# Kernel optimization log

Measured on AMD Instinct MI355X. Metric: run time of the kernel, lower is better.

The kernel has to match this reference:

```python
import jax, jax.numpy as jnp
import numpy as np

N, E, F_IN = 12288, 196608, 1433


def setup_inputs() -> dict:
    key = jax.random.key(0)
    ks = jax.random.split(key, 11)
    inp = {
        "x": jax.random.normal(ks[0], (N, F_IN), dtype=jnp.float32),
        "edge_index": jax.random.randint(ks[1], (2, E), 0, N, dtype=jnp.int64),
        "W1": jax.random.normal(ks[2], (F_IN, 32), dtype=jnp.float32) * 0.02,
        "b1": jnp.zeros((32,), dtype=jnp.float32),
        "Wl": jax.random.normal(ks[3], (32, 16), dtype=jnp.float32) * 0.1,
        "bl": jnp.zeros((16,), dtype=jnp.float32),
        "Wr": jax.random.normal(ks[4], (32, 16), dtype=jnp.float32) * 0.1,
        "br": jnp.zeros((16,), dtype=jnp.float32),
        "W3": jax.random.normal(ks[5], (16, 7), dtype=jnp.float32) * 0.1,
        "b3": jnp.zeros((7,), dtype=jnp.float32),
    }
    return inp


def reference(x, edge_index, W1, b1, Wl, bl, Wr, br, W3, b3):
    n = x.shape[0]
    loops = jnp.arange(n, dtype=edge_index.dtype)
    row = jnp.concatenate([edge_index[0], loops])  # [E+N]
    col = jnp.concatenate([edge_index[1], loops])

    # ---- GCN layer: dense symmetric-normalized adjacency (faithful to original) ----
    # degree computed over the col index of self-looped edges
    deg = jnp.zeros((n,), dtype=x.dtype).at[col].add(1.0)
    dis = jnp.where(deg > 0, deg ** -0.5, 0.0)  # inf -> 0 guard
    A = jnp.zeros((n, n), dtype=x.dtype).at[row, col].add(1.0)  # dense A-hat
    A_norm = dis[:, None] * A * dis[None, :]  # D^-1/2 A D^-1/2
    h = (A_norm @ x) @ W1 + b1
    h = jax.nn.relu(h)  # [N, 32]

    # ---- GraphSAGE layer: mean over neighbors j with edge (i -> j) ----
    src, dst = edge_index[0], edge_index[1]
    agg_sum = jax.ops.segment_sum(h[dst], src, num_segments=n)  # [N, 32]
    cnt = jax.ops.segment_sum(jnp.ones((src.shape[0],), dtype=h.dtype), src, num_segments=n)
    agg = jnp.where(cnt[:, None] > 0, agg_sum / jnp.maximum(cnt, 1.0)[:, None], 0.0)
    out = jax.nn.relu(h @ Wl + bl + agg @ Wr + br)  # [N, 16]
    out = out / (jnp.linalg.norm(out, axis=1, keepdims=True) + 1e-6)

    # ---- head: linear + dropout(eval: identity) + softmax ----
    logits = out @ W3 + b3  # [N, 7]
    return jax.nn.softmax(logits, axis=1)
```

## Files before the change

kernel.cpp:

```cpp
#include <hip/hip_runtime.h>
#include <hip/hip_bf16.h>
#include <math.h>

#define GN 12288
#define GE 196608
#define GK 1433
#define GC 32
#define CAP 64
#define NGRP 192
#define GEMMB 768
#define EDGEB 768
#define PACKB 24
#define ZEROB 96
#define XSTR 516

typedef __attribute__((ext_vector_type(8))) short bf16x8;
typedef __attribute__((ext_vector_type(4))) float f32x4;
typedef float f32x4a __attribute__((ext_vector_type(4), aligned(4)));

static __device__ inline unsigned short f2bf(float f) {
    unsigned u = __float_as_uint(f);
    return (unsigned short)((u + 0x7fffu + ((u >> 16) & 1u)) >> 16);
}
static __device__ inline float bf2f(unsigned short h) {
    return __uint_as_float(((unsigned)h) << 16);
}
static __device__ inline unsigned short f2bf_hw(float f) {
    return __builtin_bit_cast(unsigned short, __float2bfloat16(f));
}

__global__ __launch_bounds__(256) void prep_kernel(const float* __restrict__ W1,
                                                   unsigned* __restrict__ zbuf,
                                                   unsigned short* __restrict__ Whb,
                                                   unsigned short* __restrict__ Wlb) {
    int t = threadIdx.x, b = blockIdx.x;
    if (b < PACKB) {
        int idx = b * 256 + t;
        int g = idx >> 5, c = idx & 31;
        bf16x8 vh, vl;
        #pragma unroll
        for (int j = 0; j < 8; ++j) {
            int k = g * 8 + j;
            float f = (k < GK) ? W1[(size_t)k * GC + c] : 0.f;
            unsigned short hh = f2bf(f);
            vh[j] = (short)hh;
            vl[j] = (short)f2bf(f - bf2f(hh));
        }
        *(bf16x8*)(Whb + (size_t)idx * 8) = vh;
        *(bf16x8*)(Wlb + (size_t)idx * 8) = vl;
    } else {
        int idx = (b - PACKB) * 256 + t;
        zbuf[idx] = 0u;
    }
}

__global__ __launch_bounds__(256) void fused_kernel(const float* __restrict__ x,
                                                    const int* __restrict__ ei,
                                                    const unsigned short* __restrict__ Whb,
                                                    const unsigned short* __restrict__ Wlb,
                                                    float* __restrict__ xw,
                                                    unsigned* __restrict__ cnt,
                                                    unsigned* __restrict__ deg,
                                                    unsigned* __restrict__ adjF) {
    int t = threadIdx.x, bid = blockIdx.x;

    if (bid >= GEMMB) {
        int e = (bid - GEMMB) * 256 + t;
        int src = ei[e];
        int dst = ei[GE + e];
        unsigned pos = atomicAdd(&cnt[src], 1u);
        if (pos < CAP) adjF[(unsigned)src * CAP + pos] = (unsigned)dst;
        atomicAdd(&deg[dst], 1u);
        return;
    }

    __shared__ __align__(16) float xs[16][XSTR];
    int lane = t & 63, w = t >> 6;
    int quad = lane >> 4, l15 = lane & 15;
    const float* xb = x + (size_t)bid * 16 * GK;
    f32x4 acc0 = {}, acc1 = {};

    int r0 = t >> 7;
    int pos = t & 127;
    f32x4 g0, g1, g2, g3, g4, g5, g6, g7;

#define LOADG(K0) { \
    const float* pp = xb + (size_t)r0 * GK + (K0) + pos * 4; \
    g0 = *(const f32x4a*)(pp); \
    g1 = *(const f32x4a*)(pp + 2 * GK); \
    g2 = *(const f32x4a*)(pp + 4 * GK); \
    g3 = *(const f32x4a*)(pp + 6 * GK); \
    g4 = *(const f32x4a*)(pp + 8 * GK); \
    g5 = *(const f32x4a*)(pp + 10 * GK); \
    g6 = *(const f32x4a*)(pp + 12 * GK); \
    g7 = *(const f32x4a*)(pp + 14 * GK); }

#define LG1(DST, ROFF, PP, KB) { \
    const float* q_ = (PP) + (size_t)(ROFF) * GK; \
    if ((KB) + 4 <= GK) DST = *(const f32x4a*)q_; \
    else { \
        DST[0] = ((KB) + 0 < GK) ? q_[0] : 0.f; \
        DST[1] = ((KB) + 1 < GK) ? q_[1] : 0.f; \
        DST[2] = ((KB) + 2 < GK) ? q_[2] : 0.f; \
        DST[3] = ((KB) + 3 < GK) ? q_[3] : 0.f; } }

#define LOADG_TAIL(K0) { \
    const float* pp = xb + (size_t)r0 * GK + (K0) + pos * 4; \
    int kb = (K0) + pos * 4; \
    LG1(g0, 0, pp, kb)  LG1(g1, 2, pp, kb)  LG1(g2, 4, pp, kb)  LG1(g3, 6, pp, kb) \
    LG1(g4, 8, pp, kb)  LG1(g5, 10, pp, kb) LG1(g6, 12, pp, kb) LG1(g7, 14, pp, kb) }

#define STOREL() { \
    float* lp = &xs[r0][pos * 4]; \
    *(f32x4*)(lp)              = g0; \
    *(f32x4*)(lp + 2 * XSTR)   = g1; \
    *(f32x4*)(lp + 4 * XSTR)   = g2; \
    *(f32x4*)(lp + 6 * XSTR)   = g3; \
    *(f32x4*)(lp + 8 * XSTR)   = g4; \
    *(f32x4*)(lp + 10 * XSTR)  = g5; \
    *(f32x4*)(lp + 12 * XSTR)  = g6; \
    *(f32x4*)(lp + 14 * XSTR)  = g7; }

#define COMPUTE(S) { \
    _Pragma("unroll") \
    for (int c = 0; c < 4; ++c) { \
        int kl = w * 128 + c * 32 + quad * 8; \
        const float* ap = &xs[l15][kl]; \
        f32x4 x0 = *(const f32x4*)ap; \
        f32x4 x1 = *(const f32x4*)(ap + 4); \
        bf16x8 ah, al; \
        _Pragma("unroll") for (int j = 0; j < 4; ++j) { \
            unsigned short hh = f2bf_hw(x0[j]); \
            ah[j] = (short)hh; al[j] = (short)f2bf_hw(x0[j] - bf2f(hh)); } \
        _Pragma("unroll") for (int j = 0; j < 4; ++j) { \
            unsigned short hh = f2bf_hw(x1[j]); \
            ah[4 + j] = (short)hh; al[4 + j] = (short)f2bf_hw(x1[j] - bf2f(hh)); } \
        int gg = (S) * 64 + w * 16 + c * 4 + quad; \
        bf16x8 H0 = *(const bf16x8*)(Whb + (size_t)gg * 256 + l15 * 8); \
        bf16x8 H1 = *(const bf16x8*)(Whb + (size_t)gg * 256 + 128 + l15 * 8); \
        bf16x8 L0 = *(const bf16x8*)(Wlb + (size_t)gg * 256 + l15 * 8); \
        bf16x8 L1 = *(const bf16x8*)(Wlb + (size_t)gg * 256 + 128 + l15 * 8); \
        acc0 = __builtin_amdgcn_mfma_f32_16x16x32_bf16(ah, H0, acc0, 0, 0, 0); \
        acc1 = __builtin_amdgcn_mfma_f32_16x16x32_bf16(ah, H1, acc1, 0, 0, 0); \
        acc0 = __builtin_amdgcn_mfma_f32_16x16x32_bf16(ah, L0, acc0, 0, 0, 0); \
        acc1 = __builtin_amdgcn_mfma_f32_16x16x32_bf16(ah, L1, acc1, 0, 0, 0); \
        acc0 = __builtin_amdgcn_mfma_f32_16x16x32_bf16(al, H0, acc0, 0, 0, 0); \
        acc1 = __builtin_amdgcn_mfma_f32_16x16x32_bf16(al, H1, acc1, 0, 0, 0); \
    } }

    LOADG(0);
    STOREL();
    __syncthreads();
    LOADG(512);
    COMPUTE(0);
    __syncthreads();
    STOREL();
    __syncthreads();
    LOADG_TAIL(1024);
    COMPUTE(1);
    __syncthreads();
    STOREL();
    __syncthreads();
    COMPUTE(2);
    __syncthreads();

    float (*red)[16][32] = (float (*)[16][32])(&xs[0][0]);
    #pragma unroll
    for (int i = 0; i < 4; ++i) {
        red[w][quad * 4 + i][l15] = acc0[i];
        red[w][quad * 4 + i][16 + l15] = acc1[i];
    }
    __syncthreads();
    int rr0 = t >> 5, cc0 = t & 31;
    float s0 = red[0][rr0][cc0] + red[1][rr0][cc0] + red[2][rr0][cc0] + red[3][rr0][cc0];
    int rr1 = rr0 + 8;
    float s1 = red[0][rr1][cc0] + red[1][rr1][cc0] + red[2][rr1][cc0] + red[3][rr1][cc0];
    xw[(size_t)bid * 512 + t] = s0;
    xw[(size_t)bid * 512 + 256 + t] = s1;
}

__global__ __launch_bounds__(256) void gcn_kernel(const float* __restrict__ xw,
                                                  const unsigned* __restrict__ deg,
                                                  const unsigned* __restrict__ cnt,
                                                  const unsigned* __restrict__ adjF,
                                                  const float* __restrict__ b1,
                                                  float* __restrict__ h) {
    int w = threadIdx.x >> 6;
    int lane = threadIdx.x & 63;
    int i = blockIdx.x * 4 + w;
    int f = lane & 31, half = lane >> 5;
    unsigned cl = min(cnt[i], (unsigned)CAP);
    const unsigned* ai = adjF + (unsigned)i * CAP;
    float acc = 0.f;
    for (unsigned j = half; j < cl; j += 8) {
        unsigned lim = cl - 1;
        unsigned j1 = j + 2, j2 = j + 4, j3 = j + 6;
        unsigned d0 = ai[j];
        unsigned d1 = ai[min(j1, lim)];
        unsigned d2 = ai[min(j2, lim)];
        unsigned d3 = ai[min(j3, lim)];
        float m1 = j1 < cl ? 1.f : 0.f;
        float m2 = j2 < cl ? 1.f : 0.f;
        float m3 = j3 < cl ? 1.f : 0.f;
        acc += xw[(size_t)d0 * GC + f] * rsqrtf((float)(deg[d0] + 1u));
        acc += m1 * xw[(size_t)d1 * GC + f] * rsqrtf((float)(deg[d1] + 1u));
        acc += m2 * xw[(size_t)d2 * GC + f] * rsqrtf((float)(deg[d2] + 1u));
        acc += m3 * xw[(size_t)d3 * GC + f] * rsqrtf((float)(deg[d3] + 1u));
    }
    acc += __shfl_xor(acc, 32, 64);
    float disi = rsqrtf((float)(deg[i] + 1u));
    float v = b1[f] + disi * (disi * xw[(size_t)i * GC + f] + acc);
    if (half == 0) h[(size_t)i * GC + f] = fmaxf(v, 0.f);
}

__global__ __launch_bounds__(256) void sage_kernel(const float* __restrict__ h,
                                                   const unsigned* __restrict__ cnt,
                                                   const unsigned* __restrict__ adjF,
                                                   const float* __restrict__ Wl,
                                                   const float* __restrict__ bl,
                                                   const float* __restrict__ Wr,
                                                   const float* __restrict__ br,
                                                   const float* __restrict__ W3,
                                                   const float* __restrict__ b3,
                                                   float* __restrict__ out) {
    __shared__ float sh[4][64];
    __shared__ float so[4][16];
    int w = threadIdx.x >> 6, lane = threadIdx.x & 63;
    int i = blockIdx.x * 4 + w;
    int f = lane & 31, half = lane >> 5;
    unsigned ci = cnt[i];
    unsigned cl = min(ci, (unsigned)CAP);
    const unsigned* ai = adjF + (unsigned)i * CAP;
    float acc = 0.f;
    for (unsigned j = half; j < cl; j += 8) {
        unsigned lim = cl - 1;
        unsigned j1 = j + 2, j2 = j + 4, j3 = j + 6;
        unsigned d0 = ai[j];
        unsigned d1 = ai[min(j1, lim)];
        unsigned d2 = ai[min(j2, lim)];
        unsigned d3 = ai[min(j3, lim)];
        float m1 = j1 < cl ? 1.f : 0.f;
        float m2 = j2 < cl ? 1.f : 0.f;
        float m3 = j3 < cl ? 1.f : 0.f;
        acc += h[(size_t)d0 * GC + f];
        acc += m1 * h[(size_t)d1 * GC + f];
        acc += m2 * h[(size_t)d2 * GC + f];
        acc += m3 * h[(size_t)d3 * GC + f];
    }
    acc += __shfl_xor(acc, 32, 64);
    float agg = ci ? acc / (float)ci : 0.f;
    float hv = h[(size_t)i * GC + f];
    if (half == 0) { sh[w][f] = hv; sh[w][32 + f] = agg; }
    __syncthreads();
    int c = lane;
    float hid = 0.f;
    if (c < 16) {
        hid = bl[c] + br[c];
        #pragma unroll
        for (int ff = 0; ff < 32; ++ff)
            hid += sh[w][ff] * Wl[ff * 16 + c] + sh[w][32 + ff] * Wr[ff * 16 + c];
        hid = fmaxf(hid, 0.f);
    }
    float n2 = hid * hid;
    n2 += __shfl_xor(n2, 1, 64);
    n2 += __shfl_xor(n2, 2, 64);
    n2 += __shfl_xor(n2, 4, 64);
    n2 += __shfl_xor(n2, 8, 64);
    float o = hid / (sqrtf(n2) + 1e-6f);
    if (c < 16) so[w][c] = o;
    __syncthreads();
    float logit = -INFINITY;
    if (lane < 7) {
        logit = b3[lane];
        #pragma unroll
        for (int cc = 0; cc < 16; ++cc) logit += so[w][cc] * W3[cc * 7 + lane];
    }
    float m = logit;
    m = fmaxf(m, __shfl_xor(m, 1, 64));
    m = fmaxf(m, __shfl_xor(m, 2, 64));
    m = fmaxf(m, __shfl_xor(m, 4, 64));
    float e = expf(logit - m);
    float s = e;
    s += __shfl_xor(s, 1, 64);
    s += __shfl_xor(s, 2, 64);
    s += __shfl_xor(s, 4, 64);
    if (lane < 7) out[(size_t)i * 7 + lane] = e / s;
}

extern "C" void kernel_launch(void* const* d_in, const int* in_sizes, int n_in,
                              void* d_out, int out_size, void* d_ws, size_t ws_size,
                              hipStream_t stream) {
    const float* x  = (const float*)d_in[0];
    const int*   ei = (const int*)d_in[1];
    const float* W1 = (const float*)d_in[2];
    const float* b1 = (const float*)d_in[3];
    const float* Wl = (const float*)d_in[4];
    const float* bl = (const float*)d_in[5];
    const float* Wr = (const float*)d_in[6];
    const float* br = (const float*)d_in[7];
    const float* W3 = (const float*)d_in[8];
    const float* b3 = (const float*)d_in[9];
    float* out = (float*)d_out;

    char* ws = (char*)d_ws;
    const size_t S = (size_t)GN * GC * 4;
    float*    xw   = (float*)(ws);
    unsigned* cnt  = (unsigned*)(ws + S);
    unsigned* deg  = cnt + GN;
    float*    h    = (float*)(deg + GN);
    unsigned* adjF = (unsigned*)((char*)h + S);
    unsigned short* Whb = (unsigned short*)((char*)adjF + (size_t)GN * CAP * 4);
    unsigned short* Wlb = Whb + (size_t)NGRP * GC * 8;

    prep_kernel<<<PACKB + ZEROB, 256, 0, stream>>>(W1, cnt, Whb, Wlb);
    fused_kernel<<<GEMMB + EDGEB, 256, 0, stream>>>(x, ei, Whb, Wlb, xw, cnt, deg, adjF);
    gcn_kernel<<<GN / 4, 256, 0, stream>>>(xw, deg, cnt, adjF, b1, h);
    sage_kernel<<<GN / 4, 256, 0, stream>>>(h, cnt, adjF, Wl, bl, Wr, br, W3, b3, out);
}
```

Measured before the change: 154.1 us.

## Fuse edge, GEMM, GCN and SAGE stages into one cooperative kernel with grid syncs

```diff
diff --git a/kernel.cpp b/kernel.cpp
--- a/kernel.cpp
+++ b/kernel.cpp
@@ -1,6 +1,9 @@
 #include <hip/hip_runtime.h>
+#include <hip/hip_cooperative_groups.h>
 #include <hip/hip_bf16.h>
 #include <math.h>
+
+namespace cg = cooperative_groups;
 
 #define GN 12288
 #define GE 196608
@@ -13,6 +16,7 @@
 #define PACKB 24
 #define ZEROB 96
 #define XSTR 516
+#define NBLK 768
 
 typedef __attribute__((ext_vector_type(8))) short bf16x8;
 typedef __attribute__((ext_vector_type(4))) float f32x4;
@@ -29,57 +33,29 @@
     return __builtin_bit_cast(unsigned short, __float2bfloat16(f));
 }
 
-__global__ __launch_bounds__(256) void prep_kernel(const float* __restrict__ W1,
-                                                   unsigned* __restrict__ zbuf,
-                                                   unsigned short* __restrict__ Whb,
-                                                   unsigned short* __restrict__ Wlb) {
-    int t = threadIdx.x, b = blockIdx.x;
-    if (b < PACKB) {
-        int idx = b * 256 + t;
-        int g = idx >> 5, c = idx & 31;
-        bf16x8 vh, vl;
-        #pragma unroll
-        for (int j = 0; j < 8; ++j) {
-            int k = g * 8 + j;
-            float f = (k < GK) ? W1[(size_t)k * GC + c] : 0.f;
-            unsigned short hh = f2bf(f);
-            vh[j] = (short)hh;
-            vl[j] = (short)f2bf(f - bf2f(hh));
-        }
-        *(bf16x8*)(Whb + (size_t)idx * 8) = vh;
-        *(bf16x8*)(Wlb + (size_t)idx * 8) = vl;
-    } else {
-        int idx = (b - PACKB) * 256 + t;
-        zbuf[idx] = 0u;
-    }
-}
-
-__global__ __launch_bounds__(256) void fused_kernel(const float* __restrict__ x,
-                                                    const int* __restrict__ ei,
-                                                    const unsigned short* __restrict__ Whb,
-                                                    const unsigned short* __restrict__ Wlb,
-                                                    float* __restrict__ xw,
-                                                    unsigned* __restrict__ cnt,
-                                                    unsigned* __restrict__ deg,
-                                                    unsigned* __restrict__ adjF) {
-    int t = threadIdx.x, bid = blockIdx.x;
-
-    if (bid >= GEMMB) {
-        int e = (bid - GEMMB) * 256 + t;
-        int src = ei[e];
-        int dst = ei[GE + e];
-        unsigned pos = atomicAdd(&cnt[src], 1u);
-        if (pos < CAP) adjF[(unsigned)src * CAP + pos] = (unsigned)dst;
-        atomicAdd(&deg[dst], 1u);
-        return;
-    }
-
-    __shared__ __align__(16) float xs[16][XSTR];
+
+static __device__ __forceinline__ void edge_body(int e, const int* __restrict__ ei,
+                                                 unsigned* __restrict__ cnt,
+                                                 unsigned* __restrict__ deg,
+                                                 unsigned* __restrict__ adjF) {
+    int src = ei[e];
+    int dst = ei[GE + e];
+    unsigned pos = atomicAdd(&cnt[src], 1u);
+    if (pos < CAP) adjF[(unsigned)src * CAP + pos] = (unsigned)dst;
+    atomicAdd(&deg[dst], 1u);
+}
+
+static __device__ __forceinline__ void gemm_body(int bid, int t,
+                                                 const float* __restrict__ x,
+                                                 const unsigned short* __restrict__ Whb,
+                                                 const unsigned short* __restrict__ Wlb,
+                                                 float* __restrict__ xw,
+                                                 float* smem) {
     int lane = t & 63, w = t >> 6;
     int quad = lane >> 4, l15 = lane & 15;
+    float (*xs)[XSTR] = (float (*)[XSTR])smem;
     const float* xb = x + (size_t)bid * 16 * GK;
     f32x4 acc0 = {}, acc1 = {};
-
     int r0 = t >> 7;
     int pos = t & 127;
     f32x4 g0, g1, g2, g3, g4, g5, g6, g7;
@@ -164,7 +140,7 @@
     COMPUTE(2);
     __syncthreads();
 
-    float (*red)[16][32] = (float (*)[16][32])(&xs[0][0]);
+    float (*red)[16][32] = (float (*)[16][32])smem;
     #pragma unroll
     for (int i = 0; i < 4; ++i) {
         red[w][quad * 4 + i][l15] = acc0[i];
@@ -177,17 +153,20 @@
     float s1 = red[0][rr1][cc0] + red[1][rr1][cc0] + red[2][rr1][cc0] + red[3][rr1][cc0];
     xw[(size_t)bid * 512 + t] = s0;
     xw[(size_t)bid * 512 + 256 + t] = s1;
-}
-
-__global__ __launch_bounds__(256) void gcn_kernel(const float* __restrict__ xw,
-                                                  const unsigned* __restrict__ deg,
-                                                  const unsigned* __restrict__ cnt,
-                                                  const unsigned* __restrict__ adjF,
-                                                  const float* __restrict__ b1,
-                                                  float* __restrict__ h) {
-    int w = threadIdx.x >> 6;
-    int lane = threadIdx.x & 63;
-    int i = blockIdx.x * 4 + w;
+#undef LOADG
+#undef LG1
+#undef LOADG_TAIL
+#undef STOREL
+#undef COMPUTE
+}
+
+static __device__ __forceinline__ void gcn_body(int i, int lane,
+                                                const float* __restrict__ xw,
+                                                const unsigned* __restrict__ deg,
+                                                const unsigned* __restrict__ cnt,
+                                                const unsigned* __restrict__ adjF,
+                                                const float* __restrict__ b1,
+                                                float* __restrict__ h) {
     int f = lane & 31, half = lane >> 5;
     unsigned cl = min(cnt[i], (unsigned)CAP);
     const unsigned* ai = adjF + (unsigned)i * CAP;
@@ -213,20 +192,18 @@
     if (half == 0) h[(size_t)i * GC + f] = fmaxf(v, 0.f);
 }
 
-__global__ __launch_bounds__(256) void sage_kernel(const float* __restrict__ h,
-                                                   const unsigned* __restrict__ cnt,
-                                                   const unsigned* __restrict__ adjF,
-                                                   const float* __restrict__ Wl,
-                                                   const float* __restrict__ bl,
-                                                   const float* __restrict__ Wr,
-                                                   const float* __restrict__ br,
-                                                   const float* __restrict__ W3,
-                                                   const float* __restrict__ b3,
-                                                   float* __restrict__ out) {
-    __shared__ float sh[4][64];
-    __shared__ float so[4][16];
-    int w = threadIdx.x >> 6, lane = threadIdx.x & 63;
-    int i = blockIdx.x * 4 + w;
+static __device__ __forceinline__ void sage_body(int i, int w, int lane,
+                                                 float (*sh)[64], float (*so)[16],
+                                                 const float* __restrict__ h,
+                                                 const unsigned* __restrict__ cnt,
+                                                 const unsigned* __restrict__ adjF,
+                                                 const float* __restrict__ Wl,
+                                                 const float* __restrict__ bl,
+                                                 const float* __restrict__ Wr,
+                                                 const float* __restrict__ br,
+                                                 const float* __restrict__ W3,
+                                                 const float* __restrict__ b3,
+                                                 float* __restrict__ out) {
     int f = lane & 31, half = lane >> 5;
     unsigned ci = cnt[i];
     unsigned cl = min(ci, (unsigned)CAP);
@@ -279,12 +256,130 @@
     m = fmaxf(m, __shfl_xor(m, 1, 64));
     m = fmaxf(m, __shfl_xor(m, 2, 64));
     m = fmaxf(m, __shfl_xor(m, 4, 64));
-    float e = expf(logit - m);
-    float s = e;
+    float ev = expf(logit - m);
+    float s = ev;
     s += __shfl_xor(s, 1, 64);
     s += __shfl_xor(s, 2, 64);
     s += __shfl_xor(s, 4, 64);
-    if (lane < 7) out[(size_t)i * 7 + lane] = e / s;
+    if (lane < 7) out[(size_t)i * 7 + lane] = ev / s;
+}
+
+
+__global__ __launch_bounds__(256) void prep_kernel(const float* __restrict__ W1,
+                                                   unsigned* __restrict__ zbuf,
+                                                   unsigned short* __restrict__ Whb,
+                                                   unsigned short* __restrict__ Wlb) {
+    int t = threadIdx.x, b = blockIdx.x;
+    if (b < PACKB) {
+        int idx = b * 256 + t;
+        int g = idx >> 5, c = idx & 31;
+        bf16x8 vh, vl;
+        #pragma unroll
+        for (int j = 0; j < 8; ++j) {
+            int k = g * 8 + j;
+            float f = (k < GK) ? W1[(size_t)k * GC + c] : 0.f;
+            unsigned short hh = f2bf(f);
+            vh[j] = (short)hh;
+            vl[j] = (short)f2bf(f - bf2f(hh));
+        }
+        *(bf16x8*)(Whb + (size_t)idx * 8) = vh;
+        *(bf16x8*)(Wlb + (size_t)idx * 8) = vl;
+    } else {
+        int idx = (b - PACKB) * 256 + t;
+        zbuf[idx] = 0u;
+    }
+}
+
+__global__ __launch_bounds__(256) void mega3_kernel(
+    const float* __restrict__ x,
+    const int* __restrict__ ei,
+    const unsigned short* __restrict__ Whb,
+    const unsigned short* __restrict__ Wlb,
+    float* __restrict__ xw,
+    unsigned* __restrict__ cnt,
+    unsigned* __restrict__ deg,
+    unsigned* __restrict__ adjF,
+    const float* __restrict__ b1,
+    float* __restrict__ h,
+    const float* __restrict__ Wl,
+    const float* __restrict__ bl,
+    const float* __restrict__ Wr,
+    const float* __restrict__ br,
+    const float* __restrict__ W3,
+    const float* __restrict__ b3,
+    float* __restrict__ out)
+{
+    cg::grid_group grid = cg::this_grid();
+    int t = threadIdx.x, bid = blockIdx.x;
+    int lane = t & 63, w = t >> 6;
+    __shared__ __align__(16) float smem[16 * XSTR];
+
+    edge_body(bid * 256 + t, ei, cnt, deg, adjF);
+    gemm_body(bid, t, x, Whb, Wlb, xw, smem);
+
+    __threadfence_system();
+    grid.sync();
+    __threadfence_system();
+
+    #pragma unroll
+    for (int n = 0; n < 4; ++n)
+        gcn_body(bid * 16 + n * 4 + w, lane, xw, deg, cnt, adjF, b1, h);
+
+    __threadfence_system();
+    grid.sync();
+    __threadfence_system();
+
+    {
+        float (*sh)[64] = (float (*)[64])smem;
+        float (*so)[16] = (float (*)[16])(smem + 256);
+        for (int n = 0; n < 4; ++n)
+            sage_body(bid * 16 + n * 4 + w, w, lane, sh, so,
+                      h, cnt, adjF, Wl, bl, Wr, br, W3, b3, out);
+    }
+}
+
+__global__ __launch_bounds__(256) void fused_kernel(const float* __restrict__ x,
+                                                    const int* __restrict__ ei,
+                                                    const unsigned short* __restrict__ Whb,
+                                                    const unsigned short* __restrict__ Wlb,
+                                                    float* __restrict__ xw,
+                                                    unsigned* __restrict__ cnt,
+                                                    unsigned* __restrict__ deg,
+                                                    unsigned* __restrict__ adjF) {
+    int t = threadIdx.x, bid = blockIdx.x;
+    if (bid >= GEMMB) {
+        edge_body((bid - GEMMB) * 256 + t, ei, cnt, deg, adjF);
+        return;
+    }
+    __shared__ __align__(16) float smem[16 * XSTR];
+    gemm_body(bid, t, x, Whb, Wlb, xw, smem);
+}
+
+__global__ __launch_bounds__(256) void gcn_kernel(const float* __restrict__ xw,
+                                                  const unsigned* __restrict__ deg,
+                                                  const unsigned* __restrict__ cnt,
+                                                  const unsigned* __restrict__ adjF,
+                                                  const float* __restrict__ b1,
+                                                  float* __restrict__ h) {
+    int w = threadIdx.x >> 6, lane = threadIdx.x & 63;
+    gcn_body(blockIdx.x * 4 + w, lane, xw, deg, cnt, adjF, b1, h);
+}
+
+__global__ __launch_bounds__(256) void sage_kernel(const float* __restrict__ h,
+                                                   const unsigned* __restrict__ cnt,
+                                                   const unsigned* __restrict__ adjF,
+                                                   const float* __restrict__ Wl,
+                                                   const float* __restrict__ bl,
+                                                   const float* __restrict__ Wr,
+                                                   const float* __restrict__ br,
+                                                   const float* __restrict__ W3,
+                                                   const float* __restrict__ b3,
+                                                   float* __restrict__ out) {
+    __shared__ float sh[4][64];
+    __shared__ float so[4][16];
+    int w = threadIdx.x >> 6, lane = threadIdx.x & 63;
+    sage_body(blockIdx.x * 4 + w, w, lane, sh, so,
+              h, cnt, adjF, Wl, bl, Wr, br, W3, b3, out);
 }
 
 extern "C" void kernel_launch(void* const* d_in, const int* in_sizes, int n_in,
@@ -313,7 +408,20 @@
     unsigned short* Wlb = Whb + (size_t)NGRP * GC * 8;
 
     prep_kernel<<<PACKB + ZEROB, 256, 0, stream>>>(W1, cnt, Whb, Wlb);
-    fused_kernel<<<GEMMB + EDGEB, 256, 0, stream>>>(x, ei, Whb, Wlb, xw, cnt, deg, adjF);
-    gcn_kernel<<<GN / 4, 256, 0, stream>>>(xw, deg, cnt, adjF, b1, h);
-    sage_kernel<<<GN / 4, 256, 0, stream>>>(h, cnt, adjF, Wl, bl, Wr, br, W3, b3, out);
-}
+
+    void* args[] = {
+        (void*)&x, (void*)&ei, (void*)&Whb, (void*)&Wlb,
+        (void*)&xw, (void*)&cnt, (void*)&deg, (void*)&adjF,
+        (void*)&b1, (void*)&h,
+        (void*)&Wl, (void*)&bl, (void*)&Wr, (void*)&br,
+        (void*)&W3, (void*)&b3, (void*)&out
+    };
+    hipError_t err = hipLaunchCooperativeKernel((void*)mega3_kernel, dim3(NBLK),
+                                                dim3(256), args, 0, stream);
+    if (err != hipSuccess) {
+        (void)hipGetLastError();
+        fused_kernel<<<GEMMB + EDGEB, 256, 0, stream>>>(x, ei, Whb, Wlb, xw, cnt, deg, adjF);
+        gcn_kernel<<<GN / 4, 256, 0, stream>>>(xw, deg, cnt, adjF, b1, h);
+        sage_kernel<<<GN / 4, 256, 0, stream>>>(h, cnt, adjF, Wl, bl, Wr, br, W3, b3, out);
+    }
+}
```

Result: slower. 571.0 us (+270.4%).

## Aggregate edge counts in LDS histograms before global atomics

Applied to the files above, without the earlier changes.

```diff
diff --git a/kernel.cpp b/kernel.cpp
--- a/kernel.cpp
+++ b/kernel.cpp
@@ -9,7 +9,8 @@
 #define CAP 64
 #define NGRP 192
 #define GEMMB 768
-#define EDGEB 768
+#define NEDGE 8
+#define EPB   24576
 #define PACKB 24
 #define ZEROB 96
 #define XSTR 516
@@ -64,22 +65,47 @@
                                                     unsigned* __restrict__ adjF) {
     int t = threadIdx.x, bid = blockIdx.x;
 
-    if (bid >= GEMMB) {
-        int e = (bid - GEMMB) * 256 + t;
-        int src = ei[e];
-        int dst = ei[GE + e];
-        unsigned pos = atomicAdd(&cnt[src], 1u);
-        if (pos < CAP) adjF[(unsigned)src * CAP + pos] = (unsigned)dst;
-        atomicAdd(&deg[dst], 1u);
+    if (bid < NEDGE) {
+        __shared__ unsigned lc[GN];
+        __shared__ unsigned short base16[GN];
+        int e0 = bid * EPB;
+        for (int i = t; i < GN; i += 256) lc[i] = 0u;
+        __syncthreads();
+        for (int k = t; k < EPB; k += 256)
+            atomicAdd(&lc[ei[e0 + k]], 1u);
+        __syncthreads();
+        for (int i = t; i < GN; i += 256) {
+            unsigned c = lc[i];
+            if (c) base16[i] = (unsigned short)atomicAdd(&cnt[i], c);
+        }
+        __syncthreads();
+        for (int i = t; i < GN; i += 256) lc[i] = 0u;
+        __syncthreads();
+        for (int k = t; k < EPB; k += 256) {
+            int s = ei[e0 + k];
+            int d = ei[GE + e0 + k];
+            unsigned p = (unsigned)base16[s] + atomicAdd(&lc[s], 1u);
+            if (p < CAP) adjF[(unsigned)s * CAP + p] = (unsigned)d;
+        }
+        __syncthreads();
+        for (int i = t; i < GN; i += 256) lc[i] = 0u;
+        __syncthreads();
+        for (int k = t; k < EPB; k += 256)
+            atomicAdd(&lc[ei[GE + e0 + k]], 1u);
+        __syncthreads();
+        for (int i = t; i < GN; i += 256) {
+            unsigned c = lc[i];
+            if (c) atomicAdd(&deg[i], c);
+        }
         return;
     }
 
+    int gb = bid - NEDGE;
     __shared__ __align__(16) float xs[16][XSTR];
     int lane = t & 63, w = t >> 6;
     int quad = lane >> 4, l15 = lane & 15;
-    const float* xb = x + (size_t)bid * 16 * GK;
+    const float* xb = x + (size_t)gb * 16 * GK;
     f32x4 acc0 = {}, acc1 = {};
-
     int r0 = t >> 7;
     int pos = t & 127;
     f32x4 g0, g1, g2, g3, g4, g5, g6, g7;
@@ -175,8 +201,8 @@
     float s0 = red[0][rr0][cc0] + red[1][rr0][cc0] + red[2][rr0][cc0] + red[3][rr0][cc0];
     int rr1 = rr0 + 8;
     float s1 = red[0][rr1][cc0] + red[1][rr1][cc0] + red[2][rr1][cc0] + red[3][rr1][cc0];
-    xw[(size_t)bid * 512 + t] = s0;
-    xw[(size_t)bid * 512 + 256 + t] = s1;
+    xw[(size_t)gb * 512 + t] = s0;
+    xw[(size_t)gb * 512 + 256 + t] = s1;
 }
 
 __global__ __launch_bounds__(256) void gcn_kernel(const float* __restrict__ xw,
@@ -313,7 +339,7 @@
     unsigned short* Wlb = Whb + (size_t)NGRP * GC * 8;
 
     prep_kernel<<<PACKB + ZEROB, 256, 0, stream>>>(W1, cnt, Whb, Wlb);
-    fused_kernel<<<GEMMB + EDGEB, 256, 0, stream>>>(x, ei, Whb, Wlb, xw, cnt, deg, adjF);
+    fused_kernel<<<NEDGE + GEMMB, 256, 0, stream>>>(x, ei, Whb, Wlb, xw, cnt, deg, adjF);
     gcn_kernel<<<GN / 4, 256, 0, stream>>>(xw, deg, cnt, adjF, b1, h);
     sage_kernel<<<GN / 4, 256, 0, stream>>>(h, cnt, adjF, Wl, bl, Wr, br, W3, b3, out);
 }
```

Result: slower. 247.9 us (+60.9%).

## Double-buffer LDS staging of x in the GEMM with smaller K chunks

Applied to the files above, without the earlier changes.

```diff
diff --git a/kernel.cpp b/kernel.cpp
--- a/kernel.cpp
+++ b/kernel.cpp
@@ -12,7 +12,7 @@
 #define EDGEB 768
 #define PACKB 24
 #define ZEROB 96
-#define XSTR 516
+#define XSTR2 260
 
 typedef __attribute__((ext_vector_type(8))) short bf16x8;
 typedef __attribute__((ext_vector_type(4))) float f32x4;
@@ -74,26 +74,22 @@
         return;
     }
 
-    __shared__ __align__(16) float xs[16][XSTR];
+    __shared__ __align__(16) float smem[2 * 16 * XSTR2];
+    float (*xs)[16][XSTR2] = (float (*)[16][XSTR2])smem;
     int lane = t & 63, w = t >> 6;
     int quad = lane >> 4, l15 = lane & 15;
     const float* xb = x + (size_t)bid * 16 * GK;
     f32x4 acc0 = {}, acc1 = {};
-
-    int r0 = t >> 7;
-    int pos = t & 127;
-    f32x4 g0, g1, g2, g3, g4, g5, g6, g7;
-
-#define LOADG(K0) { \
-    const float* pp = xb + (size_t)r0 * GK + (K0) + pos * 4; \
-    g0 = *(const f32x4a*)(pp); \
-    g1 = *(const f32x4a*)(pp + 2 * GK); \
-    g2 = *(const f32x4a*)(pp + 4 * GK); \
-    g3 = *(const f32x4a*)(pp + 6 * GK); \
-    g4 = *(const f32x4a*)(pp + 8 * GK); \
-    g5 = *(const f32x4a*)(pp + 10 * GK); \
-    g6 = *(const f32x4a*)(pp + 12 * GK); \
-    g7 = *(const f32x4a*)(pp + 14 * GK); }
+    int r0w = t >> 6;
+    int posc = t & 63;
+    f32x4 gA0, gA1, gA2, gA3, gB0, gB1, gB2, gB3;
+
+#define LOADG(G0, G1, G2, G3, S) { \
+    const float* pp = xb + (size_t)r0w * GK + (S) * 256 + posc * 4; \
+    G0 = *(const f32x4a*)(pp); \
+    G1 = *(const f32x4a*)(pp + 4 * GK); \
+    G2 = *(const f32x4a*)(pp + 8 * GK); \
+    G3 = *(const f32x4a*)(pp + 12 * GK); }
 
 #define LG1(DST, ROFF, PP, KB) { \
     const float* q_ = (PP) + (size_t)(ROFF) * GK; \
@@ -104,28 +100,23 @@
         DST[2] = ((KB) + 2 < GK) ? q_[2] : 0.f; \
         DST[3] = ((KB) + 3 < GK) ? q_[3] : 0.f; } }
 
-#define LOADG_TAIL(K0) { \
-    const float* pp = xb + (size_t)r0 * GK + (K0) + pos * 4; \
-    int kb = (K0) + pos * 4; \
-    LG1(g0, 0, pp, kb)  LG1(g1, 2, pp, kb)  LG1(g2, 4, pp, kb)  LG1(g3, 6, pp, kb) \
-    LG1(g4, 8, pp, kb)  LG1(g5, 10, pp, kb) LG1(g6, 12, pp, kb) LG1(g7, 14, pp, kb) }
-
-#define STOREL() { \
-    float* lp = &xs[r0][pos * 4]; \
-    *(f32x4*)(lp)              = g0; \
-    *(f32x4*)(lp + 2 * XSTR)   = g1; \
-    *(f32x4*)(lp + 4 * XSTR)   = g2; \
-    *(f32x4*)(lp + 6 * XSTR)   = g3; \
-    *(f32x4*)(lp + 8 * XSTR)   = g4; \
-    *(f32x4*)(lp + 10 * XSTR)  = g5; \
-    *(f32x4*)(lp + 12 * XSTR)  = g6; \
-    *(f32x4*)(lp + 14 * XSTR)  = g7; }
-
-#define COMPUTE(S) { \
+#define LOADGT(G0, G1, G2, G3, S) { \
+    const float* pp = xb + (size_t)r0w * GK + (S) * 256 + posc * 4; \
+    int kb = (S) * 256 + posc * 4; \
+    LG1(G0, 0, pp, kb)  LG1(G1, 4, pp, kb)  LG1(G2, 8, pp, kb)  LG1(G3, 12, pp, kb) }
+
+#define STOREL(G0, G1, G2, G3, BUF) { \
+    float* lp = &xs[BUF][r0w][posc * 4]; \
+    *(f32x4*)(lp)               = G0; \
+    *(f32x4*)(lp + 4 * XSTR2)   = G1; \
+    *(f32x4*)(lp + 8 * XSTR2)   = G2; \
+    *(f32x4*)(lp + 12 * XSTR2)  = G3; }
+
+#define COMPUTE(S, BUF) { \
     _Pragma("unroll") \
-    for (int c = 0; c < 4; ++c) { \
-        int kl = w * 128 + c * 32 + quad * 8; \
-        const float* ap = &xs[l15][kl]; \
+    for (int c = 0; c < 2; ++c) { \
+        int kl = w * 64 + c * 32 + quad * 8; \
+        const float* ap = &xs[BUF][l15][kl]; \
         f32x4 x0 = *(const f32x4*)ap; \
         f32x4 x1 = *(const f32x4*)(ap + 4); \
         bf16x8 ah, al; \
@@ -135,7 +126,7 @@
         _Pragma("unroll") for (int j = 0; j < 4; ++j) { \
             unsigned short hh = f2bf_hw(x1[j]); \
             ah[4 + j] = (short)hh; al[4 + j] = (short)f2bf_hw(x1[j] - bf2f(hh)); } \
-        int gg = (S) * 64 + w * 16 + c * 4 + quad; \
+        int gg = (S) * 32 + w * 8 + c * 4 + quad; \
         bf16x8 H0 = *(const bf16x8*)(Whb + (size_t)gg * 256 + l15 * 8); \
         bf16x8 H1 = *(const bf16x8*)(Whb + (size_t)gg * 256 + 128 + l15 * 8); \
         bf16x8 L0 = *(const bf16x8*)(Wlb + (size_t)gg * 256 + l15 * 8); \
@@ -148,23 +139,32 @@
         acc1 = __builtin_amdgcn_mfma_f32_16x16x32_bf16(al, H1, acc1, 0, 0, 0); \
     } }
 
-    LOADG(0);
-    STOREL();
-    __syncthreads();
-    LOADG(512);
-    COMPUTE(0);
-    __syncthreads();
-    STOREL();
-    __syncthreads();
-    LOADG_TAIL(1024);
-    COMPUTE(1);
-    __syncthreads();
-    STOREL();
-    __syncthreads();
-    COMPUTE(2);
-    __syncthreads();
-
-    float (*red)[16][32] = (float (*)[16][32])(&xs[0][0]);
+    LOADG(gA0, gA1, gA2, gA3, 0);
+    STOREL(gA0, gA1, gA2, gA3, 0);
+    LOADG(gB0, gB1, gB2, gB3, 1);
+    __syncthreads();
+    LOADG(gA0, gA1, gA2, gA3, 2);
+    COMPUTE(0, 0);
+    STOREL(gB0, gB1, gB2, gB3, 1);
+    __syncthreads();
+    LOADG(gB0, gB1, gB2, gB3, 3);
+    COMPUTE(1, 1);
+    STOREL(gA0, gA1, gA2, gA3, 0);
+    __syncthreads();
+    LOADG(gA0, gA1, gA2, gA3, 4);
+    COMPUTE(2, 0);
+    STOREL(gB0, gB1, gB2, gB3, 1);
+    __syncthreads();
+    LOADGT(gB0, gB1, gB2, gB3, 5);
+    COMPUTE(3, 1);
+    STOREL(gA0, gA1, gA2, gA3, 0);
+    __syncthreads();
+    COMPUTE(4, 0);
+    STOREL(gB0, gB1, gB2, gB3, 1);
+    __syncthreads();
+    COMPUTE(5, 1);
+
+    float (*red)[16][32] = (float (*)[16][32])smem;
     #pragma unroll
     for (int i = 0; i < 4; ++i) {
         red[w][quad * 4 + i][l15] = acc0[i];
```

Result: no change. 153.6 us (-0.3%).
